# Optimization experiments

Hardware: AMD Instinct MI355X
Metric: run time of the kernel (lower is better)

## Reference

```python
import jax, jax.numpy as jnp
import numpy as np

N_HEAD = 12
LN_EPS = 1e-5


def _layernorm(x, g, b):
    m = jnp.mean(x, axis=-1, keepdims=True)
    v = jnp.mean(jnp.square(x - m), axis=-1, keepdims=True)
    return (x - m) * jax.lax.rsqrt(v + LN_EPS) * g + b


def _block(x, p):
    # p holds single-layer params. x: [B, S, D]
    B, S, D = x.shape
    Dh = D // N_HEAD
    h = _layernorm(x, p['ln1_g'], p['ln1_b'])
    q = (h @ p['wq'] + p['bq']).reshape(B, S, N_HEAD, Dh)
    k = (h @ p['wk'] + p['bk']).reshape(B, S, N_HEAD, Dh)
    v = (h @ p['wv'] + p['bv']).reshape(B, S, N_HEAD, Dh)
    scores = jnp.einsum('bqhd,bkhd->bhqk', q, k) / np.sqrt(Dh).astype(x.dtype)
    causal = jnp.tril(jnp.ones((S, S), dtype=bool))  # valid_nums = arange(1..S)
    scores = jnp.where(causal, scores, -jnp.inf)
    attn = jax.nn.softmax(scores, axis=-1)  # dropout is identity in eval
    o = jnp.einsum('bhqk,bkhd->bqhd', attn, v).reshape(B, S, D)
    x = x + o @ p['wo'] + p['bo']
    h2 = _layernorm(x, p['ln2_g'], p['ln2_b'])
    ff = jax.nn.gelu(h2 @ p['w1'] + p['b1'], approximate=False) @ p['w2'] + p['b2']
    return x + ff


def _gpt_forward(idx, wte, wpe, layer_params, lnf_g, lnf_b, lm_w):
    S = idx.shape[1]
    x = wte[idx] + wpe[None, :S, :]  # embd dropout is identity in eval
    x = jax.lax.scan(lambda c, p: (_block(c, p), None), x, layer_params)[0]
    x = _layernorm(x, lnf_g, lnf_b)
    return x @ lm_w  # logits [B, S, V]


def setup_inputs() -> dict:
    B, S, D, V, L, F = 4, 1024, 768, 50257, 12, 3072
    key = jax.random.key(0)
    ks = iter(jax.random.split(key, 24))
    std = 0.02
    std_proj = 0.02 / np.sqrt(2 * L)  # special init for w_o / FFN.linear2

    def w(shape, s=std):
        return jax.random.normal(next(ks), shape, jnp.float32) * s

    return dict(
        idx=jax.random.randint(next(ks), (B, S), 0, V),
        wte=w((V, D)), wpe=w((S, D)),
        ln1_g=jnp.ones((L, D)), ln1_b=jnp.zeros((L, D)),
        wq=w((L, D, D)), bq=jnp.zeros((L, D)),
        wk=w((L, D, D)), bk=jnp.zeros((L, D)),
        wv=w((L, D, D)), bv=jnp.zeros((L, D)),
        wo=w((L, D, D), std_proj), bo=jnp.zeros((L, D)),
        ln2_g=jnp.ones((L, D)), ln2_b=jnp.zeros((L, D)),
        w1=w((L, D, F)), b1=jnp.zeros((L, F)),
        w2=w((L, F, D), std_proj), b2=jnp.zeros((L, D)),
        lnf_g=jnp.ones((D,)), lnf_b=jnp.zeros((D,)),
        lm_w=w((D, V)),
    )


def reference(idx, wte, wpe, ln1_g, ln1_b, wq, bq, wk, bk, wv, bv, wo, bo,
              ln2_g, ln2_b, w1, b1, w2, b2, lnf_g, lnf_b, lm_w):
    layer_params = dict(ln1_g=ln1_g, ln1_b=ln1_b, wq=wq, bq=bq, wk=wk, bk=bk,
                        wv=wv, bv=bv, wo=wo, bo=bo, ln2_g=ln2_g, ln2_b=ln2_b,
                        w1=w1, b1=b1, w2=w2, b2=b2)
    return _gpt_forward(idx, wte, wpe, layer_params, lnf_g, lnf_b, lm_w)
```

## Files before the change

### kernel.cpp

```cpp
#include <hip/hip_runtime.h>
#include <hip/hip_bf16.h>

typedef __attribute__((ext_vector_type(8))) short short8;
typedef __attribute__((ext_vector_type(4))) short short4v;
typedef __attribute__((ext_vector_type(4))) float floatx4;

#define GLD16(g, l) __builtin_amdgcn_global_load_lds( \
    (__attribute__((address_space(1))) void*)(g),      \
    (__attribute__((address_space(3))) void*)(l), 16, 0, 0)

#define MFMA_BF16(a, b, c) __builtin_amdgcn_mfma_f32_16x16x32_bf16((a), (b), (c), 0, 0, 0)

__device__ __forceinline__ short f2bf(float f) {
  union { __hip_bfloat16 h; short s; } u;
  u.h = __float2bfloat16(f);
  return u.s;
}

__global__ __launch_bounds__(256)
void transpose_convert(const float* __restrict__ in, short* __restrict__ out,
                       const int K, const int N, const size_t inStride,
                       const size_t outStride) {
  in += blockIdx.z * inStride;
  out += blockIdx.z * outStride;
  __shared__ float tile[32][33];
  const int n0 = blockIdx.x * 32;
  const int k0 = blockIdx.y * 32;
  const int tx = threadIdx.x;
  const int ty = threadIdx.y;
#pragma unroll
  for (int i = 0; i < 4; ++i) {
    const int kk = ty + i * 8;
    const int nn = n0 + tx;
    tile[kk][tx] = (nn < N) ? in[(size_t)(k0 + kk) * N + nn] : 0.f;
  }
  __syncthreads();
#pragma unroll
  for (int i = 0; i < 4; ++i) {
    const int nn = ty + i * 8;
    out[(size_t)(n0 + nn) * K + k0 + tx] = f2bf(tile[tx][nn]);
  }
}

__global__ __launch_bounds__(256)
void embed_kernel(const int* __restrict__ idx, const float* __restrict__ wte,
                  const float* __restrict__ wpe, float* __restrict__ x) {
  const int row = blockIdx.x;
  const int tok = idx[row];
  const int s = row & 1023;
  const float* wt = wte + (size_t)tok * 768;
  const float* wp = wpe + (size_t)s * 768;
  float* xr = x + (size_t)row * 768;
  for (int c = threadIdx.x; c < 768; c += 256) xr[c] = wt[c] + wp[c];
}

__global__ __launch_bounds__(256)
void ln_kernel(const float* __restrict__ x, const float* __restrict__ g,
               const float* __restrict__ b, short* __restrict__ out) {
  const int wv = threadIdx.x >> 6, lane = threadIdx.x & 63;
  const int row = blockIdx.x * 4 + wv;
  const float* xr = x + (size_t)row * 768 + lane * 12;
  const float4 a0 = *(const float4*)(xr);
  const float4 a1 = *(const float4*)(xr + 4);
  const float4 a2 = *(const float4*)(xr + 8);
  float v[12] = {a0.x, a0.y, a0.z, a0.w, a1.x, a1.y, a1.z, a1.w,
                 a2.x, a2.y, a2.z, a2.w};
  float s = 0.f;
#pragma unroll
  for (int i = 0; i < 12; ++i) s += v[i];
#pragma unroll
  for (int m = 1; m < 64; m <<= 1) s += __shfl_xor(s, m);
  const float mean = s * (1.0f / 768.0f);
  float q = 0.f;
#pragma unroll
  for (int i = 0; i < 12; ++i) {
    v[i] -= mean;
    q += v[i] * v[i];
  }
#pragma unroll
  for (int m = 1; m < 64; m <<= 1) q += __shfl_xor(q, m);
  const float inv = rsqrtf(q * (1.0f / 768.0f) + 1e-5f);

  const float* gp = g + lane * 12;
  const float* bp = b + lane * 12;
  const float4 g0 = *(const float4*)(gp);
  const float4 g1 = *(const float4*)(gp + 4);
  const float4 g2 = *(const float4*)(gp + 8);
  const float4 b0 = *(const float4*)(bp);
  const float4 b1 = *(const float4*)(bp + 4);
  const float4 b2 = *(const float4*)(bp + 8);
  const float gg[12] = {g0.x, g0.y, g0.z, g0.w, g1.x, g1.y, g1.z, g1.w,
                        g2.x, g2.y, g2.z, g2.w};
  const float bb[12] = {b0.x, b0.y, b0.z, b0.w, b1.x, b1.y, b1.z, b1.w,
                        b2.x, b2.y, b2.z, b2.w};
  short r[12];
#pragma unroll
  for (int i = 0; i < 12; ++i) r[i] = f2bf(v[i] * inv * gg[i] + bb[i]);
  short* orow = out + (size_t)row * 768 + lane * 12;
#pragma unroll
  for (int i = 0; i < 3; ++i)
    *(short4v*)(orow + i * 4) = short4v{r[i * 4], r[i * 4 + 1], r[i * 4 + 2],
                                        r[i * 4 + 3]};
}

enum { EPI_QKV = 0, EPI_RESID = 1, EPI_GELU = 2 };

template <int BM, int BN, int DBUF, int EPI>
__global__ __launch_bounds__(256)
void gemm_kernel(const short* __restrict__ A, const short* __restrict__ Bt,
                 const int K,
                 const float* __restrict__ bias0, const float* __restrict__ bias1,
                 const float* __restrict__ bias2, float* __restrict__ fout,
                 short* __restrict__ bout0, short* __restrict__ bout1,
                 short* __restrict__ bout2) {
  constexpr int MF = BM / 32;
  constexpr int NF = BN / 32;
  __shared__ short sA[DBUF + 1][BM * 64];
  __shared__ short sB[DBUF + 1][BN * 64];
  const int tid = threadIdx.x;
  const int wv = tid >> 6;
  const int lane = tid & 63;
  const int lrow = lane & 15;
  const int lk8 = lane >> 4;
  const int m0 = blockIdx.x * BM;
  const int n0 = blockIdx.y * BN;
  const int wm = (wv >> 1) * (BM / 2);
  const int wn = (wv & 1) * (BN / 2);
  constexpr int MW = BM / 2 / 16;
  constexpr int NW = BN / 2 / 16;

  floatx4 acc[MW][NW];
#pragma unroll
  for (int m = 0; m < MW; ++m)
#pragma unroll
    for (int n = 0; n < NW; ++n) acc[m][n] = {0.f, 0.f, 0.f, 0.f};

  const short* pA[MF];
  const short* pB[NF];
#pragma unroll
  for (int i = 0; i < MF; ++i) {
    const int p = i * 256 + tid;
    const int rr = p >> 3, up = p & 7;
    pA[i] = A + (size_t)(m0 + rr) * K + ((up ^ (rr & 7)) << 3);
  }
#pragma unroll
  for (int i = 0; i < NF; ++i) {
    const int p = i * 256 + tid;
    const int rr = p >> 3, up = p & 7;
    pB[i] = Bt + (size_t)(n0 + rr) * K + ((up ^ (rr & 7)) << 3);
  }

  auto stage = [&](int buf) {
#pragma unroll
    for (int i = 0; i < MF; ++i) {
      GLD16(pA[i], sA[buf] + (i * 256 + wv * 64) * 8);
      pA[i] += 64;
    }
#pragma unroll
    for (int i = 0; i < NF; ++i) {
      GLD16(pB[i], sB[buf] + (i * 256 + wv * 64) * 8);
      pB[i] += 64;
    }
  };

  auto compute = [&](const short* pa, const short* pb) {
    const int xr = lrow & 7;
    short8 af[MW][2], bv[NW][2];
#pragma unroll
    for (int m = 0; m < MW; ++m) {
      const int row = (wm + m * 16 + lrow) * 64;
      af[m][0] = *(const short8*)(pa + row + ((lk8 ^ xr) << 3));
      af[m][1] = *(const short8*)(pa + row + (((4 + lk8) ^ xr) << 3));
    }
#pragma unroll
    for (int n = 0; n < NW; ++n) {
      const int row = (wn + n * 16 + lrow) * 64;
      bv[n][0] = *(const short8*)(pb + row + ((lk8 ^ xr) << 3));
      bv[n][1] = *(const short8*)(pb + row + (((4 + lk8) ^ xr) << 3));
    }
#pragma unroll
    for (int m = 0; m < MW; ++m)
#pragma unroll
      for (int n = 0; n < NW; ++n) {
        acc[m][n] = MFMA_BF16(af[m][0], bv[n][0], acc[m][n]);
        acc[m][n] = MFMA_BF16(af[m][1], bv[n][1], acc[m][n]);
      }
  };

  const int nk = K >> 6;
  if (DBUF) {
    stage(0);
    __syncthreads();
    int cur = 0;
    for (int kt = 0; kt < nk; ++kt) {
      if (kt + 1 < nk) stage(cur ^ 1);
      compute(sA[cur], sB[cur]);
      __syncthreads();
      cur ^= 1;
    }
  } else {
    for (int kt = 0; kt < nk; ++kt) {
      stage(0);
      __syncthreads();
      compute(sA[0], sB[0]);
      __syncthreads();
    }
  }

#pragma unroll
  for (int m = 0; m < MW; ++m) {
#pragma unroll
    for (int n = 0; n < NW; ++n) {
#pragma unroll
      for (int r = 0; r < 4; ++r) {
        const float v = acc[m][n][r];
        const int gm = m0 + wm + m * 16 + lk8 * 4 + r;
        const int gn = n0 + wn + n * 16 + lrow;
        if (EPI == EPI_QKV) {
          const int sec = (gn >= 1536) ? 2 : (gn >= 768 ? 1 : 0);
          const int nn = gn - sec * 768;
          const int hh = nn >> 6, dh = nn & 63;
          const int bb = gm >> 10, srow = gm & 1023;
          if (sec == 0) {
            bout0[(((size_t)(bb * 12 + hh) * 1024 + srow) << 6) + dh] =
                f2bf((v + bias0[nn]) * 0.18033688f);
          } else if (sec == 1) {
            bout1[(((size_t)(bb * 12 + hh) * 1024 + srow) << 6) + dh] =
                f2bf(v + bias1[nn]);
          } else {
            bout2[(((size_t)(bb * 12 + hh) * 64 + dh) << 10) + srow] =
                f2bf(v + bias2[nn]);
          }
        } else if (EPI == EPI_RESID) {
          float* xp = fout + (size_t)gm * 768 + gn;
          *xp = *xp + v + bias0[gn];
        } else {
          const float tt = v + bias0[gn];
          const float gl = 0.5f * tt * (1.f + erff(tt * 0.70710678118654752f));
          bout0[(size_t)gm * 3072 + gn] = f2bf(gl);
        }
      }
    }
  }
}

__global__ __launch_bounds__(512, 4)
void gemm_lm_kernel(const short* __restrict__ A, const short* __restrict__ Bt,
                    float* __restrict__ fout) {
  __shared__ short sA[256 * 64];
  __shared__ short sB[128 * 64];
  const int K = 768;
  const int tid = threadIdx.x;
  const int wv = tid >> 6;
  const int lane = tid & 63;
  const int lrow = lane & 15;
  const int lk8 = lane >> 4;
  const int m0 = blockIdx.x * 256;
  const int n0 = blockIdx.y * 128;
  const int wm = (wv >> 1) * 64;
  const int wn = (wv & 1) * 64;

  floatx4 acc[4][4];
#pragma unroll
  for (int m = 0; m < 4; ++m)
#pragma unroll
    for (int n = 0; n < 4; ++n) acc[m][n] = {0.f, 0.f, 0.f, 0.f};

  const short* Ab = A + (size_t)m0 * K;
  const short* Bb = Bt + (size_t)n0 * K;

  const short* pA[4];
  const short* pB[2];
#pragma unroll
  for (int i = 0; i < 4; ++i) {
    const int p = i * 512 + tid;
    const int rr = p >> 3, up = p & 7;
    pA[i] = Ab + (size_t)rr * K + ((up ^ (rr & 7)) << 3);
  }
#pragma unroll
  for (int i = 0; i < 2; ++i) {
    const int p = i * 512 + tid;
    const int rr = p >> 3, up = p & 7;
    pB[i] = Bb + (size_t)rr * K + ((up ^ (rr & 7)) << 3);
  }

  const int arow = (wm + lrow) * 64;
  const int xr = (lrow & 7);

  for (int kt = 0; kt < 12; ++kt) {
#pragma unroll
    for (int i = 0; i < 4; ++i) {
      GLD16(pA[i], sA + (i * 512 + wv * 64) * 8);
      pA[i] += 64;
    }
#pragma unroll
    for (int i = 0; i < 2; ++i) {
      GLD16(pB[i], sB + (i * 512 + wv * 64) * 8);
      pB[i] += 64;
    }
    __syncthreads();

    short8 bvv[4][2];
#pragma unroll
    for (int n = 0; n < 4; ++n) {
      const int brow = (wn + n * 16 + lrow) * 64;
      bvv[n][0] = *(const short8*)(sB + brow + ((lk8 ^ xr) << 3));
      bvv[n][1] = *(const short8*)(sB + brow + (((4 + lk8) ^ xr) << 3));
    }
#pragma unroll
    for (int m = 0; m < 4; ++m) {
      const short8 a0 = *(const short8*)(sA + arow + m * 1024 + ((lk8 ^ xr) << 3));
      const short8 a1 =
          *(const short8*)(sA + arow + m * 1024 + (((4 + lk8) ^ xr) << 3));
#pragma unroll
      for (int n = 0; n < 4; ++n) {
        acc[m][n] = MFMA_BF16(a0, bvv[n][0], acc[m][n]);
        acc[m][n] = MFMA_BF16(a1, bvv[n][1], acc[m][n]);
      }
    }
    __syncthreads();
  }

#pragma unroll
  for (int m = 0; m < 4; ++m)
#pragma unroll
    for (int n = 0; n < 4; ++n)
#pragma unroll
      for (int r = 0; r < 4; ++r) {
        const int gm = m0 + wm + m * 16 + lk8 * 4 + r;
        const int gn = n0 + wn + n * 16 + lrow;
        if (gn < 50257) fout[(size_t)gm * 50257 + gn] = acc[m][n][r];
      }
}

__global__ __launch_bounds__(256)
void attn_kernel(const short* __restrict__ q, const short* __restrict__ k,
                 const short* __restrict__ vt, short* __restrict__ o) {
  __shared__ short sK[64 * 64];
  __shared__ short sV[64 * 64];
  const int bh = blockIdx.x;
  const int qi = 15 - blockIdx.y;
  const int tid = threadIdx.x;
  const int wv = tid >> 6, lane = tid & 63;
  const int lrow = lane & 15, lk8 = lane >> 4;
  const int q0 = qi * 64;
  const int qrow = q0 + wv * 16 + lrow;

  const short* qg = q + ((size_t)(bh * 1024 + qrow)) * 64 + lk8 * 8;
  const short8 qf0 = *(const short8*)qg;
  const short8 qf1 = *(const short8*)(qg + 32);

  float m_run = -1e30f, lsum = 0.f;
  floatx4 accO[4];
#pragma unroll
  for (int n = 0; n < 4; ++n) accO[n] = {0.f, 0.f, 0.f, 0.f};

  for (int t = 0; t <= qi; ++t) {
    const int k0 = t * 64;
#pragma unroll
    for (int i = 0; i < 2; ++i) {
      const int e = (i * 256 + tid) * 8;
      const int r = e >> 6, cc = e & 63;
      const int su = ((cc >> 3) ^ (r & 7)) << 3;
      *(short8*)(sK + r * 64 + su) =
          *(const short8*)(k + ((size_t)(bh * 1024 + k0 + r)) * 64 + cc);
      *(short8*)(sV + r * 64 + su) =
          *(const short8*)(vt + ((size_t)(bh * 64 + r)) * 1024 + k0 + cc);
    }
    __syncthreads();

    floatx4 accS[4];
#pragma unroll
    for (int n = 0; n < 4; ++n) accS[n] = {0.f, 0.f, 0.f, 0.f};
    const int rKb = ((lrow >> 2) << 3) + (lrow & 3);
#pragma unroll
    for (int ks = 0; ks < 2; ++ks) {
      const short8 qf = ks ? qf1 : qf0;
#pragma unroll
      for (int n = 0; n < 4; ++n) {
        const int rK = ((n >> 1) << 5) + ((n & 1) << 2) + rKb;
        const short8 kf =
            *(const short8*)(sK + rK * 64 + (((ks * 4 + lk8) ^ (rK & 7)) << 3));
        accS[n] = MFMA_BF16(kf, qf, accS[n]);
      }
    }

    float sv[4][4];
    float mx = -1e30f;
#pragma unroll
    for (int n = 0; n < 4; ++n)
#pragma unroll
      for (int r = 0; r < 4; ++r) {
        const int key = k0 + ((n >> 1) << 5) + (lk8 << 3) + ((n & 1) << 2) + r;
        float s = accS[n][r];
        s = (key > qrow) ? -1e30f : s;
        sv[n][r] = s;
        mx = fmaxf(mx, s);
      }
    mx = fmaxf(mx, __shfl_xor(mx, 16));
    mx = fmaxf(mx, __shfl_xor(mx, 32));
    const float mnew = fmaxf(m_run, mx);
    const float sf = exp2f(m_run - mnew);
    m_run = mnew;

    float rs = 0.f;
    unsigned int w[4][2];
#pragma unroll
    for (int n = 0; n < 4; ++n)
#pragma unroll
      for (int rp = 0; rp < 2; ++rp) {
        const float ea = exp2f(sv[n][2 * rp] - mnew);
        const float eb = exp2f(sv[n][2 * rp + 1] - mnew);
        rs += ea + eb;
        w[n][rp] = (unsigned int)(unsigned short)f2bf(ea) |
                   ((unsigned int)(unsigned short)f2bf(eb) << 16);
      }
    lsum = lsum * sf + rs;

    float sfq[4];
#pragma unroll
    for (int r = 0; r < 4; ++r)
      sfq[r] = __shfl(sf, (lane & 48) | (lk8 * 4 + r));
#pragma unroll
    for (int n = 0; n < 4; ++n)
#pragma unroll
      for (int r = 0; r < 4; ++r) accO[n][r] *= sfq[r];

    union { short8 s; unsigned int u[4]; } paf0, paf1;
#pragma unroll
    for (int tt = 0; tt < 4; ++tt) {
      paf0.u[tt] = w[tt >> 1][tt & 1];
      paf1.u[tt] = w[2 + (tt >> 1)][tt & 1];
    }

#pragma unroll
    for (int n = 0; n < 4; ++n) {
      const int dh = n * 16 + lrow;
      const short8 vf0 = *(const short8*)(sV + dh * 64 + ((lk8 ^ (dh & 7)) << 3));
      const short8 vf1 =
          *(const short8*)(sV + dh * 64 + (((4 + lk8) ^ (dh & 7)) << 3));
      accO[n] = MFMA_BF16(paf0.s, vf0, accO[n]);
      accO[n] = MFMA_BF16(paf1.s, vf1, accO[n]);
    }
    __syncthreads();
  }

  float ls = lsum;
  ls += __shfl_xor(ls, 16);
  ls += __shfl_xor(ls, 32);
  const float invown = 1.f / ls;
  float invq[4];
#pragma unroll
  for (int r = 0; r < 4; ++r)
    invq[r] = __shfl(invown, (lane & 48) | (lk8 * 4 + r));

  const int bb = bh / 12, hh = bh % 12;
#pragma unroll
  for (int n = 0; n < 4; ++n)
#pragma unroll
    for (int r = 0; r < 4; ++r) {
      const int row = q0 + wv * 16 + lk8 * 4 + r;
      const float ov = accO[n][r] * invq[r];
      o[((size_t)(bb * 1024 + row)) * 768 + hh * 64 + n * 16 + lrow] = f2bf(ov);
    }
}

extern "C" void kernel_launch(void* const* d_in, const int* in_sizes, int n_in,
                              void* d_out, int out_size, void* d_ws, size_t ws_size,
                              hipStream_t stream) {
  const int* idx = (const int*)d_in[0];
  const float* wte = (const float*)d_in[1];
  const float* wpe = (const float*)d_in[2];
  const float* ln1_g = (const float*)d_in[3];
  const float* ln1_b = (const float*)d_in[4];
  const float* wq = (const float*)d_in[5];
  const float* bq = (const float*)d_in[6];
  const float* wk = (const float*)d_in[7];
  const float* bk = (const float*)d_in[8];
  const float* wv = (const float*)d_in[9];
  const float* bv = (const float*)d_in[10];
  const float* wo = (const float*)d_in[11];
  const float* bo = (const float*)d_in[12];
  const float* ln2_g = (const float*)d_in[13];
  const float* ln2_b = (const float*)d_in[14];
  const float* w1 = (const float*)d_in[15];
  const float* b1 = (const float*)d_in[16];
  const float* w2 = (const float*)d_in[17];
  const float* b2 = (const float*)d_in[18];
  const float* lnf_g = (const float*)d_in[19];
  const float* lnf_b = (const float*)d_in[20];
  const float* lm_w = (const float*)d_in[21];
  float* out = (float*)d_out;

  char* base = (char*)d_ws;
  size_t off = 0;
  auto alloc = [&](size_t bytes) {
    char* r = base + off;
    off = (off + bytes + 255) & ~(size_t)255;
    return r;
  };
  short* lmT = (short*)alloc((size_t)50304 * 768 * 2);
  float* x = (float*)alloc((size_t)4096 * 768 * 4);
  short* h = (short*)alloc((size_t)4096 * 768 * 2);
  short* qb = (short*)alloc((size_t)4096 * 768 * 2);
  short* kb = (short*)alloc((size_t)4096 * 768 * 2);
  short* vtb = (short*)alloc((size_t)4096 * 768 * 2);
  short* ob = (short*)alloc((size_t)4096 * 768 * 2);
  short* ff = (short*)alloc((size_t)4096 * 3072 * 2);

  const size_t LW = 7077888;
  const size_t dd = (size_t)768 * 768;
  const bool big = (off + (size_t)12 * LW * 2 + 256 <= ws_size);
  short* wAll = nullptr;
  short *wqkvT = nullptr, *woT = nullptr, *w1T = nullptr, *w2T = nullptr;
  if (big) {
    wAll = (short*)alloc((size_t)12 * LW * 2);
  } else {
    wqkvT = (short*)alloc((size_t)2304 * 768 * 2);
    woT = (short*)alloc((size_t)768 * 768 * 2);
    w1T = (short*)alloc((size_t)3072 * 768 * 2);
    w2T = (short*)alloc((size_t)768 * 3072 * 2);
    if (off > ws_size) return;
  }

  const dim3 tb(32, 8);
  transpose_convert<<<dim3(1572, 24, 1), tb, 0, stream>>>(lm_w, lmT, 768, 50257, 0, 0);
  if (big) {
    transpose_convert<<<dim3(24, 24, 12), tb, 0, stream>>>(wq, wAll + 0, 768, 768, dd, LW);
    transpose_convert<<<dim3(24, 24, 12), tb, 0, stream>>>(wk, wAll + 589824, 768, 768, dd, LW);
    transpose_convert<<<dim3(24, 24, 12), tb, 0, stream>>>(wv, wAll + 1179648, 768, 768, dd, LW);
    transpose_convert<<<dim3(24, 24, 12), tb, 0, stream>>>(wo, wAll + 1769472, 768, 768, dd, LW);
    transpose_convert<<<dim3(96, 24, 12), tb, 0, stream>>>(w1, wAll + 2359296, 768, 3072,
                                                           (size_t)768 * 3072, LW);
    transpose_convert<<<dim3(24, 96, 12), tb, 0, stream>>>(w2, wAll + 4718592, 3072, 768,
                                                           (size_t)3072 * 768, LW);
  }
  embed_kernel<<<4096, 256, 0, stream>>>(idx, wte, wpe, x);

  for (int l = 0; l < 12; ++l) {
    const short *pQKV, *pWO, *pW1, *pW2;
    if (big) {
      short* wl = wAll + (size_t)l * LW;
      pQKV = wl;
      pWO = wl + 1769472;
      pW1 = wl + 2359296;
      pW2 = wl + 4718592;
    } else {
      transpose_convert<<<dim3(24, 24, 1), tb, 0, stream>>>(wq + l * dd, wqkvT, 768, 768, 0, 0);
      transpose_convert<<<dim3(24, 24, 1), tb, 0, stream>>>(wk + l * dd, wqkvT + dd, 768, 768, 0, 0);
      transpose_convert<<<dim3(24, 24, 1), tb, 0, stream>>>(wv + l * dd, wqkvT + 2 * dd, 768, 768, 0, 0);
      transpose_convert<<<dim3(24, 24, 1), tb, 0, stream>>>(wo + l * dd, woT, 768, 768, 0, 0);
      transpose_convert<<<dim3(96, 24, 1), tb, 0, stream>>>(w1 + (size_t)l * 768 * 3072, w1T, 768, 3072, 0, 0);
      transpose_convert<<<dim3(24, 96, 1), tb, 0, stream>>>(w2 + (size_t)l * 3072 * 768, w2T, 3072, 768, 0, 0);
      pQKV = wqkvT; pWO = woT; pW1 = w1T; pW2 = w2T;
    }

    ln_kernel<<<1024, 256, 0, stream>>>(x, ln1_g + l * 768, ln1_b + l * 768, h);
    gemm_kernel<128, 64, 1, EPI_QKV><<<dim3(32, 36), 256, 0, stream>>>(
        h, pQKV, 768, bq + l * 768, bk + l * 768, bv + l * 768, nullptr, qb, kb, vtb);
    attn_kernel<<<dim3(48, 16), 256, 0, stream>>>(qb, kb, vtb, ob);
    gemm_kernel<64, 64, 1, EPI_RESID><<<dim3(64, 12), 256, 0, stream>>>(
        ob, pWO, 768, bo + l * 768, nullptr, nullptr, x, nullptr, nullptr, nullptr);
    ln_kernel<<<1024, 256, 0, stream>>>(x, ln2_g + l * 768, ln2_b + l * 768, h);
    gemm_kernel<128, 64, 1, EPI_GELU><<<dim3(32, 48), 256, 0, stream>>>(
        h, pW1, 768, b1 + l * 3072, nullptr, nullptr, nullptr, ff, nullptr, nullptr);
    gemm_kernel<64, 64, 1, EPI_RESID><<<dim3(64, 12), 256, 0, stream>>>(
        ff, pW2, 3072, b2 + l * 768, nullptr, nullptr, x, nullptr, nullptr, nullptr);
  }

  ln_kernel<<<1024, 256, 0, stream>>>(x, lnf_g, lnf_b, h);
  gemm_lm_kernel<<<dim3(16, 393), 512, 0, stream>>>(h, lmT, out);
}
```

Baseline: 2.828 ms.

## Double-buffer K/V tiles in attention and skip softmax rescale when max is stable

The attention kernel now keeps two shared-memory buffers for K and V. It prefetches the next tile into registers while computing on the current one, then writes it into the other buffer, so each iteration needs only one barrier. It also adds a lazy rescale: when every lane's new max stays within 8 (log2 units) of the running max, the exp2 rescale and the accumulator multiply are skipped. The costs are extra LDS and registers per block, and exponentials can grow up to 2^8 against a stale max, which loosens the bf16 precision margin on P.

```diff
diff --git a/kernel.cpp b/kernel.cpp
--- a/kernel.cpp
+++ b/kernel.cpp
@@ -336,8 +336,8 @@
 __global__ __launch_bounds__(256)
 void attn_kernel(const short* __restrict__ q, const short* __restrict__ k,
                  const short* __restrict__ vt, short* __restrict__ o) {
-  __shared__ short sK[64 * 64];
-  __shared__ short sV[64 * 64];
+  __shared__ short sK[2][64 * 64];
+  __shared__ short sV[2][64 * 64];
   const int bh = blockIdx.x;
   const int qi = 15 - blockIdx.y;
   const int tid = threadIdx.x;
@@ -350,29 +350,48 @@
   const short8 qf0 = *(const short8*)qg;
   const short8 qf1 = *(const short8*)(qg + 32);
 
+  const int e0 = tid * 8, e1 = (256 + tid) * 8;
+  const int sr0 = e0 >> 6, sc0 = e0 & 63;
+  const int sr1 = e1 >> 6, sc1 = e1 & 63;
+  const int su0 = ((sc0 >> 3) ^ (sr0 & 7)) << 3;
+  const int su1 = ((sc1 >> 3) ^ (sr1 & 7)) << 3;
+  const short* kb = k + (size_t)bh * 1024 * 64;
+  const short* vb = vt + (size_t)bh * 64 * 1024;
+
+  short8 kreg0, kreg1, vreg0, vreg1;
+  auto load_tile = [&](int k0) {
+    kreg0 = *(const short8*)(kb + (size_t)(k0 + sr0) * 64 + sc0);
+    kreg1 = *(const short8*)(kb + (size_t)(k0 + sr1) * 64 + sc1);
+    vreg0 = *(const short8*)(vb + (size_t)sr0 * 1024 + k0 + sc0);
+    vreg1 = *(const short8*)(vb + (size_t)sr1 * 1024 + k0 + sc1);
+  };
+  auto write_tile = [&](short* dK, short* dV) {
+    *(short8*)(dK + sr0 * 64 + su0) = kreg0;
+    *(short8*)(dK + sr1 * 64 + su1) = kreg1;
+    *(short8*)(dV + sr0 * 64 + su0) = vreg0;
+    *(short8*)(dV + sr1 * 64 + su1) = vreg1;
+  };
+
   float m_run = -1e30f, lsum = 0.f;
   floatx4 accO[4];
 #pragma unroll
   for (int n = 0; n < 4; ++n) accO[n] = {0.f, 0.f, 0.f, 0.f};
 
+  load_tile(0);
+  write_tile(sK[0], sV[0]);
+  __syncthreads();
+
+  int cur = 0;
   for (int t = 0; t <= qi; ++t) {
     const int k0 = t * 64;
-#pragma unroll
-    for (int i = 0; i < 2; ++i) {
-      const int e = (i * 256 + tid) * 8;
-      const int r = e >> 6, cc = e & 63;
-      const int su = ((cc >> 3) ^ (r & 7)) << 3;
-      *(short8*)(sK + r * 64 + su) =
-          *(const short8*)(k + ((size_t)(bh * 1024 + k0 + r)) * 64 + cc);
-      *(short8*)(sV + r * 64 + su) =
-          *(const short8*)(vt + ((size_t)(bh * 64 + r)) * 1024 + k0 + cc);
-    }
-    __syncthreads();
+    if (t < qi) load_tile(k0 + 64);
 
     floatx4 accS[4];
 #pragma unroll
     for (int n = 0; n < 4; ++n) accS[n] = {0.f, 0.f, 0.f, 0.f};
     const int rKb = ((lrow >> 2) << 3) + (lrow & 3);
+    const short* pK = sK[cur];
+    const short* pV = sV[cur];
 #pragma unroll
     for (int ks = 0; ks < 2; ++ks) {
       const short8 qf = ks ? qf1 : qf0;
@@ -380,7 +399,7 @@
       for (int n = 0; n < 4; ++n) {
         const int rK = ((n >> 1) << 5) + ((n & 1) << 2) + rKb;
         const short8 kf =
-            *(const short8*)(sK + rK * 64 + (((ks * 4 + lk8) ^ (rK & 7)) << 3));
+            *(const short8*)(pK + rK * 64 + (((ks * 4 + lk8) ^ (rK & 7)) << 3));
         accS[n] = MFMA_BF16(kf, qf, accS[n]);
       }
     }
@@ -399,9 +418,14 @@
       }
     mx = fmaxf(mx, __shfl_xor(mx, 16));
     mx = fmaxf(mx, __shfl_xor(mx, 32));
-    const float mnew = fmaxf(m_run, mx);
-    const float sf = exp2f(m_run - mnew);
-    m_run = mnew;
+
+    const bool skip = __all(mx <= m_run + 8.0f);
+    float sf = 1.f;
+    if (!skip) {
+      const float mnew = fmaxf(m_run, mx);
+      sf = exp2f(m_run - mnew);
+      m_run = mnew;
+    }
 
     float rs = 0.f;
     unsigned int w[4][2];
@@ -409,22 +433,26 @@
     for (int n = 0; n < 4; ++n)
 #pragma unroll
       for (int rp = 0; rp < 2; ++rp) {
-        const float ea = exp2f(sv[n][2 * rp] - mnew);
-        const float eb = exp2f(sv[n][2 * rp + 1] - mnew);
+        const float ea = exp2f(sv[n][2 * rp] - m_run);
+        const float eb = exp2f(sv[n][2 * rp + 1] - m_run);
         rs += ea + eb;
         w[n][rp] = (unsigned int)(unsigned short)f2bf(ea) |
                    ((unsigned int)(unsigned short)f2bf(eb) << 16);
       }
-    lsum = lsum * sf + rs;
-
-    float sfq[4];
-#pragma unroll
-    for (int r = 0; r < 4; ++r)
-      sfq[r] = __shfl(sf, (lane & 48) | (lk8 * 4 + r));
-#pragma unroll
-    for (int n = 0; n < 4; ++n)
-#pragma unroll
-      for (int r = 0; r < 4; ++r) accO[n][r] *= sfq[r];
+
+    if (skip) {
+      lsum += rs;
+    } else {
+      lsum = lsum * sf + rs;
+      float sfq[4];
+#pragma unroll
+      for (int r = 0; r < 4; ++r)
+        sfq[r] = __shfl(sf, (lane & 48) | (lk8 * 4 + r));
+#pragma unroll
+      for (int n = 0; n < 4; ++n)
+#pragma unroll
+        for (int r = 0; r < 4; ++r) accO[n][r] *= sfq[r];
+    }
 
     union { short8 s; unsigned int u[4]; } paf0, paf1;
 #pragma unroll
@@ -436,13 +464,16 @@
 #pragma unroll
     for (int n = 0; n < 4; ++n) {
       const int dh = n * 16 + lrow;
-      const short8 vf0 = *(const short8*)(sV + dh * 64 + ((lk8 ^ (dh & 7)) << 3));
+      const short8 vf0 = *(const short8*)(pV + dh * 64 + ((lk8 ^ (dh & 7)) << 3));
       const short8 vf1 =
-          *(const short8*)(sV + dh * 64 + (((4 + lk8) ^ (dh & 7)) << 3));
+          *(const short8*)(pV + dh * 64 + (((4 + lk8) ^ (dh & 7)) << 3));
       accO[n] = MFMA_BF16(paf0.s, vf0, accO[n]);
       accO[n] = MFMA_BF16(paf1.s, vf1, accO[n]);
     }
+
+    if (t < qi) write_tile(sK[cur ^ 1], sV[cur ^ 1]);
     __syncthreads();
+    cur ^= 1;
   }
 
   float ls = lsum;
```

Result: no change. 2.829 ms (+0.0%).
